# Optimization experiments

Measured on AMD Instinct MI355X. Metric: run time of the kernel, lower is better.

## Reference

```python
import jax, jax.numpy as jnp
import numpy as np

B, A, C = 16, 3, 80
N = 200
SCALES = (80, 40, 20)
BOX_W, OBJ_W, CLS_W = 7.5, 1.0, 0.5


def setup_inputs() -> dict:
    key = jax.random.key(0)
    ks = jax.random.split(key, 6)
    preds = {}
    for i, s in enumerate(SCALES):
        preds[f"pred{i}"] = jax.random.normal(ks[i], (B, A, s, s, 5 + C), dtype=jnp.float32)
    b_idx = jax.random.randint(ks[3], (N,), 0, B).astype(jnp.float32)
    cls_idx = jax.random.randint(ks[4], (N,), 0, C).astype(jnp.float32)
    xywh = jax.random.uniform(ks[5], (N, 4), dtype=jnp.float32)
    targets = jnp.concatenate([b_idx[:, None], cls_idx[:, None], xywh], axis=1)
    return {**preds, "targets": targets}


def _bce_with_logits_mean(logits, z):
    # mean( max(x,0) - x*z + log(1+exp(-|x|)) ) == mean( logaddexp(0,x) - x*z )
    return jnp.mean(jnp.logaddexp(jnp.float32(0.0), logits) - logits * z)


def reference(pred0, pred1, pred2, targets):
    preds = (pred0, pred1, pred2)
    # filter targets with class >= num_classes (mask instead of dynamic shape)
    valid = targets[:, 1] < C                       # [N] bool
    val = valid.astype(jnp.float32)                 # 1.0 for valid rows
    b = jnp.where(valid, targets[:, 0].astype(jnp.int32), 0)
    cl = jnp.where(valid, targets[:, 1].astype(jnp.int32), 0)
    x, y = targets[:, 2], targets[:, 3]

    total_obj = jnp.float32(0.0)
    total_cls = jnp.float32(0.0)
    for pred in preds:
        _, _, H, W, _ = pred.shape
        gx = jnp.minimum(jnp.floor(x * W).astype(jnp.int32), W - 1)
        gy = jnp.minimum(jnp.floor(y * H).astype(jnp.int32), H - 1)
        # scatter 1.0 at (b, anchor 0, gy, gx); .max handles duplicates & masked rows
        obj_t = jnp.zeros((B, A, H, W), jnp.float32).at[b, 0, gy, gx].max(val)
        cls_t = jnp.zeros((B, A, H, W, C), jnp.float32).at[b, 0, gy, gx, cl].max(val)
        total_obj = total_obj + _bce_with_logits_mean(pred[..., 4], obj_t)
        total_cls = total_cls + _bce_with_logits_mean(pred[..., 5:], cls_t)

    total_box = jnp.float32(0.0)  # box loss never accumulated in source
    total = BOX_W * total_box + OBJ_W * total_obj + CLS_W * total_cls
    return jnp.stack([total, total_box, total_obj, total_cls])
```

## Files before the change

### kernel.cpp

```cpp
#include <hip/hip_runtime.h>

namespace {

constexpr int Cn = 80, NTGT = 200;
constexpr unsigned CH = 85;
constexpr unsigned S0 = 80, S1 = 40, S2 = 20;

constexpr unsigned F0 = 16u * 3u * 80u * 80u * 85u / 4u;
constexpr unsigned F1 = 16u * 3u * 40u * 40u * 85u / 4u;
constexpr unsigned F2 = 16u * 3u * 20u * 20u * 85u / 4u;

constexpr unsigned BLOCK = 256;
constexpr unsigned NBLK  = 2048;
constexpr unsigned STRIDE = NBLK * BLOCK;
constexpr unsigned CSTEP  = (STRIDE * 4u) % CH;

constexpr float WO0 = 1.0f / (48.0f * 80.0f * 80.0f);
constexpr float WO1 = 1.0f / (48.0f * 40.0f * 40.0f);
constexpr float WO2 = 1.0f / (48.0f * 20.0f * 20.0f);
constexpr float WC0 = WO0 / 80.0f;
constexpr float WC1 = WO1 / 80.0f;
constexpr float WC2 = WO2 / 80.0f;

__device__ __forceinline__ float softplus_lean(float x) {
    float s = fminf(fabsf(x) * 1.44269504f, 30.0f);
    int   n = (int)s;
    float f = s - (float)n;
    float q = fmaf(fmaf(0.171122f, f, -0.668647f), f, 0.998651f);
    float e2 = __int_as_float((127 - n) << 23);
    float u  = q * e2;
    float p  = u * fmaf(fmaf(0.118988f, u, -0.415863f), u, 0.990022f);
    return fmaxf(x, 0.0f) + p;
}

__device__ __forceinline__ void proc4(const float4 v, unsigned c0,
                                      float& accO, float& accC)
{
    float vals[4] = {v.x, v.y, v.z, v.w};
    #pragma unroll
    for (unsigned k = 0; k < 4; ++k) {
        float sp = softplus_lean(vals[k]);
        accC += ((c0 - (5u - k)) < 80u) ? sp : 0.0f;
        accO += (c0 == (4u - k))        ? sp : 0.0f;
    }
}

__device__ __forceinline__ unsigned wrap85(unsigned c) {
    return (c >= CH) ? c - CH : c;
}

__global__ __launch_bounds__(BLOCK) void yolo_sum_kernel(
    const float* __restrict__ p0, const float* __restrict__ p1,
    const float* __restrict__ p2, float2* __restrict__ part)
{
    unsigned tid = blockIdx.x * BLOCK + threadIdx.x;
    unsigned c0_init = (tid * 4u) % CH;

    float totO = 0.0f, totC = 0.0f;

    {
        const float4* P = (const float4*)p0;
        float accO = 0.0f, accC = 0.0f;
        unsigned c0 = c0_init;
        for (unsigned i = tid; i < F0; i += STRIDE) {
            proc4(P[i], c0, accO, accC);
            c0 = wrap85(c0 + CSTEP);
        }
        totO = fmaf(WO0, accO, totO); totC = fmaf(WC0, accC, totC);
    }
    {
        const float4* P = (const float4*)p1;
        float accO = 0.0f, accC = 0.0f;
        unsigned c0 = c0_init;
        for (unsigned i = tid; i < F1; i += STRIDE) {
            proc4(P[i], c0, accO, accC);
            c0 = wrap85(c0 + CSTEP);
        }
        totO = fmaf(WO1, accO, totO); totC = fmaf(WC1, accC, totC);
    }
    {
        const float4* P = (const float4*)p2;
        float accO = 0.0f, accC = 0.0f;
        unsigned c0 = c0_init;
        for (unsigned i = tid; i < F2; i += STRIDE) {
            proc4(P[i], c0, accO, accC);
            c0 = wrap85(c0 + CSTEP);
        }
        totO = fmaf(WO2, accO, totO); totC = fmaf(WC2, accC, totC);
    }

    #pragma unroll
    for (int off = 32; off > 0; off >>= 1) {
        totO += __shfl_down(totO, off);
        totC += __shfl_down(totC, off);
    }
    __shared__ float sO[4], sC[4];
    int lane = threadIdx.x & 63, wv = threadIdx.x >> 6;
    if (lane == 0) { sO[wv] = totO; sC[wv] = totC; }
    __syncthreads();
    if (threadIdx.x == 0)
        part[blockIdx.x] = make_float2(sO[0] + sO[1] + sO[2] + sO[3],
                                       sC[0] + sC[1] + sC[2] + sC[3]);
}

__global__ __launch_bounds__(BLOCK) void yolo_corr_final_kernel(
    const float* __restrict__ p0, const float* __restrict__ p1,
    const float* __restrict__ p2, const float* __restrict__ tgt,
    const float2* __restrict__ part, float* __restrict__ out)
{
    __shared__ unsigned keyO[NTGT], keyC[NTGT];

    int t = threadIdx.x;
    float fb = 0.f, fc = 0.f, fx = 0.f, fy = 0.f;
    bool valid = false;
    if (t < NTGT) {
        fb = tgt[t * 6 + 0];
        fc = tgt[t * 6 + 1];
        fx = tgt[t * 6 + 2];
        fy = tgt[t * 6 + 3];
        valid = (fc < (float)Cn);
    }
    int b  = valid ? (int)fb : 0;
    int cl = valid ? (int)fc : 0;

    const float* preds[3] = {p0, p1, p2};
    const int    SS[3]    = {(int)S0, (int)S1, (int)S2};
    const float  WOs[3]   = {WO0, WO1, WO2};
    const float  WCs[3]   = {WC0, WC1, WC2};

    float accO = 0.0f, accC = 0.0f;

    for (int s = 0; s < 3; ++s) {
        int W = SS[s];
        unsigned myO = 0x80000000u | (unsigned)t;
        unsigned myC = myO;
        float vObj = 0.f, vCls = 0.f;
        if (t < NTGT && valid) {
            int gx = min((int)floorf(fx * (float)W), W - 1);
            int gy = min((int)floorf(fy * (float)W), W - 1);
            myO = ((unsigned)b << 14) | ((unsigned)gy << 7) | (unsigned)gx;
            myC = (myO << 7) | (unsigned)cl;
            const float* P = preds[s];
            unsigned cell = ((unsigned)b * 3u * (unsigned)W + (unsigned)gy)
                            * (unsigned)W + (unsigned)gx;
            vObj = P[cell * CH + 4u];
            vCls = P[cell * CH + 5u + (unsigned)cl];
        }
        if (t < NTGT) { keyO[t] = myO; keyC[t] = myC; }
        __syncthreads();

        bool uo = true, uc = true;
        int lim = (t < NTGT) ? t : 0;
        #pragma unroll 4
        for (int j = 0; j < lim; ++j) {
            unsigned ko = keyO[j], kc = keyC[j];
            uo = uo && (ko != myO);
            uc = uc && (kc != myC);
        }
        if (t < NTGT && valid) {
            if (uo) accO -= vObj * WOs[s];
            if (uc) accC -= vCls * WCs[s];
        }
        __syncthreads();
    }

    for (unsigned i = threadIdx.x; i < NBLK; i += BLOCK) {
        float2 pp = part[i];
        accO += pp.x; accC += pp.y;
    }

    #pragma unroll
    for (int off = 32; off > 0; off >>= 1) {
        accO += __shfl_down(accO, off);
        accC += __shfl_down(accC, off);
    }
    __shared__ float rO[4], rC[4];
    int lane = threadIdx.x & 63, wv = threadIdx.x >> 6;
    if (lane == 0) { rO[wv] = accO; rC[wv] = accC; }
    __syncthreads();
    if (threadIdx.x == 0) {
        float obj = rO[0] + rO[1] + rO[2] + rO[3];
        float cls = rC[0] + rC[1] + rC[2] + rC[3];
        out[0] = obj + 0.5f * cls;
        out[1] = 0.0f;
        out[2] = obj;
        out[3] = cls;
    }
}

}

extern "C" void kernel_launch(void* const* d_in, const int* in_sizes, int n_in,
                              void* d_out, int out_size, void* d_ws, size_t ws_size,
                              hipStream_t stream)
{
    const float* p0  = (const float*)d_in[0];
    const float* p1  = (const float*)d_in[1];
    const float* p2  = (const float*)d_in[2];
    const float* tgt = (const float*)d_in[3];
    float* out = (float*)d_out;
    float2* part = (float2*)d_ws;

    yolo_sum_kernel       <<<NBLK, BLOCK, 0, stream>>>(p0, p1, p2, part);
    yolo_corr_final_kernel<<<1,    BLOCK, 0, stream>>>(p0, p1, p2, tgt, part, out);
}
```

Measured before the change: 49.40 us.

## Fuse sum and correction kernels into one launch with atomic last-block finalize

Merges the streaming softplus-sum kernel and the single-block target-correction/final-reduction kernel into one launch, where an extra block handles the target corrections and the last block to finish writes the output using float atomics and a completion counter. This removes the second kernel launch and the serial 2048-entry partial reduction. It also adds software prefetching of the next float4 in the streaming loops and specializes the smallest scale to a single load. The cost is a memset launch for the accumulators, plus 2049 float atomics whose ordering is nondeterministic.

```diff
diff --git a/kernel.cpp b/kernel.cpp
--- a/kernel.cpp
+++ b/kernel.cpp
@@ -49,124 +49,107 @@
     return (c >= CH) ? c - CH : c;
 }
 
-__global__ __launch_bounds__(BLOCK) void yolo_sum_kernel(
-    const float* __restrict__ p0, const float* __restrict__ p1,
-    const float* __restrict__ p2, float2* __restrict__ part)
-{
-    unsigned tid = blockIdx.x * BLOCK + threadIdx.x;
-    unsigned c0_init = (tid * 4u) % CH;
-
-    float totO = 0.0f, totC = 0.0f;
-
-    {
-        const float4* P = (const float4*)p0;
-        float accO = 0.0f, accC = 0.0f;
-        unsigned c0 = c0_init;
-        for (unsigned i = tid; i < F0; i += STRIDE) {
-            proc4(P[i], c0, accO, accC);
-            c0 = wrap85(c0 + CSTEP);
-        }
-        totO = fmaf(WO0, accO, totO); totC = fmaf(WC0, accC, totC);
-    }
-    {
-        const float4* P = (const float4*)p1;
-        float accO = 0.0f, accC = 0.0f;
-        unsigned c0 = c0_init;
-        for (unsigned i = tid; i < F1; i += STRIDE) {
-            proc4(P[i], c0, accO, accC);
-            c0 = wrap85(c0 + CSTEP);
-        }
-        totO = fmaf(WO1, accO, totO); totC = fmaf(WC1, accC, totC);
-    }
-    {
-        const float4* P = (const float4*)p2;
-        float accO = 0.0f, accC = 0.0f;
-        unsigned c0 = c0_init;
-        for (unsigned i = tid; i < F2; i += STRIDE) {
-            proc4(P[i], c0, accO, accC);
-            c0 = wrap85(c0 + CSTEP);
-        }
-        totO = fmaf(WO2, accO, totO); totC = fmaf(WC2, accC, totC);
-    }
-
-    #pragma unroll
-    for (int off = 32; off > 0; off >>= 1) {
-        totO += __shfl_down(totO, off);
-        totC += __shfl_down(totC, off);
-    }
-    __shared__ float sO[4], sC[4];
-    int lane = threadIdx.x & 63, wv = threadIdx.x >> 6;
-    if (lane == 0) { sO[wv] = totO; sC[wv] = totC; }
-    __syncthreads();
-    if (threadIdx.x == 0)
-        part[blockIdx.x] = make_float2(sO[0] + sO[1] + sO[2] + sO[3],
-                                       sC[0] + sC[1] + sC[2] + sC[3]);
-}
-
-__global__ __launch_bounds__(BLOCK) void yolo_corr_final_kernel(
+__global__ __launch_bounds__(BLOCK) void yolo_fused_kernel(
     const float* __restrict__ p0, const float* __restrict__ p1,
     const float* __restrict__ p2, const float* __restrict__ tgt,
-    const float2* __restrict__ part, float* __restrict__ out)
+    float* __restrict__ acc, unsigned* __restrict__ counter,
+    float* __restrict__ out)
 {
     __shared__ unsigned keyO[NTGT], keyC[NTGT];
-
-    int t = threadIdx.x;
-    float fb = 0.f, fc = 0.f, fx = 0.f, fy = 0.f;
-    bool valid = false;
-    if (t < NTGT) {
-        fb = tgt[t * 6 + 0];
-        fc = tgt[t * 6 + 1];
-        fx = tgt[t * 6 + 2];
-        fy = tgt[t * 6 + 3];
-        valid = (fc < (float)Cn);
-    }
-    int b  = valid ? (int)fb : 0;
-    int cl = valid ? (int)fc : 0;
-
-    const float* preds[3] = {p0, p1, p2};
-    const int    SS[3]    = {(int)S0, (int)S1, (int)S2};
-    const float  WOs[3]   = {WO0, WO1, WO2};
-    const float  WCs[3]   = {WC0, WC1, WC2};
-
     float accO = 0.0f, accC = 0.0f;
 
-    for (int s = 0; s < 3; ++s) {
-        int W = SS[s];
-        unsigned myO = 0x80000000u | (unsigned)t;
-        unsigned myC = myO;
-        float vObj = 0.f, vCls = 0.f;
-        if (t < NTGT && valid) {
-            int gx = min((int)floorf(fx * (float)W), W - 1);
-            int gy = min((int)floorf(fy * (float)W), W - 1);
-            myO = ((unsigned)b << 14) | ((unsigned)gy << 7) | (unsigned)gx;
-            myC = (myO << 7) | (unsigned)cl;
-            const float* P = preds[s];
-            unsigned cell = ((unsigned)b * 3u * (unsigned)W + (unsigned)gy)
-                            * (unsigned)W + (unsigned)gx;
-            vObj = P[cell * CH + 4u];
-            vCls = P[cell * CH + 5u + (unsigned)cl];
-        }
-        if (t < NTGT) { keyO[t] = myO; keyC[t] = myC; }
-        __syncthreads();
-
-        bool uo = true, uc = true;
-        int lim = (t < NTGT) ? t : 0;
-        #pragma unroll 4
-        for (int j = 0; j < lim; ++j) {
-            unsigned ko = keyO[j], kc = keyC[j];
-            uo = uo && (ko != myO);
-            uc = uc && (kc != myC);
-        }
-        if (t < NTGT && valid) {
-            if (uo) accO -= vObj * WOs[s];
-            if (uc) accC -= vCls * WCs[s];
-        }
-        __syncthreads();
-    }
-
-    for (unsigned i = threadIdx.x; i < NBLK; i += BLOCK) {
-        float2 pp = part[i];
-        accO += pp.x; accC += pp.y;
+    if (blockIdx.x < NBLK) {
+        unsigned tid = blockIdx.x * BLOCK + threadIdx.x;
+        unsigned c0i = (tid * 4u) % CH;
+
+        {
+            const float4* P = (const float4*)p0;
+            float aO = 0.f, aC = 0.f; unsigned c0 = c0i;
+            if (tid < F0) {
+                float4 nxt = P[tid];
+                for (unsigned j = tid + STRIDE; j < F0; j += STRIDE) {
+                    float4 cur = nxt;
+                    nxt = P[j];
+                    proc4(cur, c0, aO, aC);
+                    c0 = wrap85(c0 + CSTEP);
+                }
+                proc4(nxt, c0, aO, aC);
+            }
+            accO = fmaf(WO0, aO, accO); accC = fmaf(WC0, aC, accC);
+        }
+        {
+            const float4* P = (const float4*)p1;
+            float aO = 0.f, aC = 0.f; unsigned c0 = c0i;
+            if (tid < F1) {
+                float4 nxt = P[tid];
+                for (unsigned j = tid + STRIDE; j < F1; j += STRIDE) {
+                    float4 cur = nxt;
+                    nxt = P[j];
+                    proc4(cur, c0, aO, aC);
+                    c0 = wrap85(c0 + CSTEP);
+                }
+                proc4(nxt, c0, aO, aC);
+            }
+            accO = fmaf(WO1, aO, accO); accC = fmaf(WC1, aC, accC);
+        }
+        if (tid < F2) {
+            const float4* P = (const float4*)p2;
+            float aO = 0.f, aC = 0.f;
+            proc4(P[tid], c0i, aO, aC);
+            accO = fmaf(WO2, aO, accO); accC = fmaf(WC2, aC, accC);
+        }
+    } else {
+        int t = threadIdx.x;
+        float fb = 0.f, fc = 0.f, fx = 0.f, fy = 0.f;
+        bool valid = false;
+        if (t < NTGT) {
+            fb = tgt[t * 6 + 0];
+            fc = tgt[t * 6 + 1];
+            fx = tgt[t * 6 + 2];
+            fy = tgt[t * 6 + 3];
+            valid = (fc < (float)Cn);
+        }
+        int b  = valid ? (int)fb : 0;
+        int cl = valid ? (int)fc : 0;
+
+        const float* preds[3] = {p0, p1, p2};
+        const int    SS[3]    = {(int)S0, (int)S1, (int)S2};
+        const float  WOs[3]   = {WO0, WO1, WO2};
+        const float  WCs[3]   = {WC0, WC1, WC2};
+
+        for (int s = 0; s < 3; ++s) {
+            int W = SS[s];
+            unsigned myO = 0x80000000u | (unsigned)t;
+            unsigned myC = myO;
+            float vObj = 0.f, vCls = 0.f;
+            if (t < NTGT && valid) {
+                int gx = min((int)floorf(fx * (float)W), W - 1);
+                int gy = min((int)floorf(fy * (float)W), W - 1);
+                myO = ((unsigned)b << 14) | ((unsigned)gy << 7) | (unsigned)gx;
+                myC = (myO << 7) | (unsigned)cl;
+                const float* P = preds[s];
+                unsigned cell = ((unsigned)b * 3u * (unsigned)W + (unsigned)gy)
+                                * (unsigned)W + (unsigned)gx;
+                vObj = P[cell * CH + 4u];
+                vCls = P[cell * CH + 5u + (unsigned)cl];
+            }
+            if (t < NTGT) { keyO[t] = myO; keyC[t] = myC; }
+            __syncthreads();
+
+            bool uo = true, uc = true;
+            int lim = (t < NTGT) ? t : 0;
+            #pragma unroll 4
+            for (int j = 0; j < lim; ++j) {
+                unsigned ko = keyO[j], kc = keyC[j];
+                uo = uo && (ko != myO);
+                uc = uc && (kc != myC);
+            }
+            if (t < NTGT && valid) {
+                if (uo) accO -= vObj * WOs[s];
+                if (uc) accC -= vCls * WCs[s];
+            }
+            __syncthreads();
+        }
     }
 
     #pragma unroll
@@ -174,17 +157,29 @@
         accO += __shfl_down(accO, off);
         accC += __shfl_down(accC, off);
     }
-    __shared__ float rO[4], rC[4];
+    __shared__ float sO[4], sC[4];
     int lane = threadIdx.x & 63, wv = threadIdx.x >> 6;
-    if (lane == 0) { rO[wv] = accO; rC[wv] = accC; }
+    if (lane == 0) { sO[wv] = accO; sC[wv] = accC; }
     __syncthreads();
+
     if (threadIdx.x == 0) {
-        float obj = rO[0] + rO[1] + rO[2] + rO[3];
-        float cls = rC[0] + rC[1] + rC[2] + rC[3];
-        out[0] = obj + 0.5f * cls;
-        out[1] = 0.0f;
-        out[2] = obj;
-        out[3] = cls;
+        float o = sO[0] + sO[1] + sO[2] + sO[3];
+        float c = sC[0] + sC[1] + sC[2] + sC[3];
+        atomicAdd(&acc[0], o);
+        atomicAdd(&acc[1], c);
+        __threadfence();
+        unsigned old = atomicAdd(counter, 1u);
+        if (old == NBLK) {
+            __threadfence();
+            float obj = __hip_atomic_load(&acc[0], __ATOMIC_RELAXED,
+                                          __HIP_MEMORY_SCOPE_AGENT);
+            float cls = __hip_atomic_load(&acc[1], __ATOMIC_RELAXED,
+                                          __HIP_MEMORY_SCOPE_AGENT);
+            out[0] = obj + 0.5f * cls;
+            out[1] = 0.0f;
+            out[2] = obj;
+            out[3] = cls;
+        }
     }
 }
 
@@ -199,8 +194,11 @@
     const float* p2  = (const float*)d_in[2];
     const float* tgt = (const float*)d_in[3];
     float* out = (float*)d_out;
-    float2* part = (float2*)d_ws;
-
-    yolo_sum_kernel       <<<NBLK, BLOCK, 0, stream>>>(p0, p1, p2, part);
-    yolo_corr_final_kernel<<<1,    BLOCK, 0, stream>>>(p0, p1, p2, tgt, part, out);
-}
+
+    float*    acc     = (float*)d_ws;
+    unsigned* counter = (unsigned*)((char*)d_ws + 8);
+
+    hipMemsetAsync(d_ws, 0, 12, stream);
+    yolo_fused_kernel<<<NBLK + 1, BLOCK, 0, stream>>>(p0, p1, p2, tgt,
+                                                      acc, counter, out);
+}
```

Result: slower. 106.0 us (median of 2 runs) (+114.5%).
